# Performance work log

Measured on AMD Instinct MI355X. Metric: run time of the kernel, lower is better.

The kernel has to match this reference:

```python
import jax, jax.numpy as jnp
import numpy as np

B, LQ, D, H, L, P, DFF = 16, 1024, 256, 8, 4, 4, 1024
SHAPES = ((64, 64), (32, 32), (16, 16), (8, 8))  # (H_l, W_l) per level
LV = sum(h * w for h, w in SHAPES)  # 5440
DH = D // H
EPS = 1e-5


def layer_norm(x, g, b):
    m = jnp.mean(x, -1, keepdims=True)
    v = jnp.mean((x - m) ** 2, -1, keepdims=True)
    return (x - m) * jax.lax.rsqrt(v + EPS) * g + b


def mha(q_in, k_in, v_in, w, b, ow, ob):
    # torch nn.MultiheadAttention with packed in_proj [3D, D]
    q = (q_in @ w[:D].T + b[:D]).reshape(B, LQ, H, DH)
    k = (k_in @ w[D:2 * D].T + b[D:2 * D]).reshape(B, LQ, H, DH)
    v = (v_in @ w[2 * D:].T + b[2 * D:]).reshape(B, LQ, H, DH)
    a = jax.nn.softmax(jnp.einsum('bqhd,bkhd->bhqk', q, k) * (1.0 / np.sqrt(DH)), -1)
    o = jnp.einsum('bhqk,bkhd->bqhd', a, v).reshape(B, LQ, D)
    return o @ ow.T + ob


def ms_deform_attn(q, ref, src, value_w, value_b, off_w, off_b, attw_w, attw_b, outp_w, outp_b):
    # value: [B, H, LV, DH]
    value = (src @ value_w.T + value_b).reshape(B, LV, H, DH).transpose(0, 2, 1, 3)
    off = (q @ off_w.T + off_b).reshape(B, LQ, H, L, P, 2)
    attw = jax.nn.softmax((q @ attw_w.T + attw_b).reshape(B, LQ, H, L * P), -1).reshape(B, LQ, H, L, P)
    # offset normalizer = (W_l, H_l) matching (x, y) order of reference points
    normalizer = jnp.array([[w, h] for h, w in SHAPES], jnp.float32)
    loc = ref[:, :, None, :, None, :] + off / normalizer[None, None, None, :, None, :]  # [B,LQ,H,L,P,2]
    out = jnp.zeros((B, LQ, H, DH), jnp.float32)
    start = 0
    for l, (hl, wl) in enumerate(SHAPES):
        v = value[:, :, start:start + hl * wl]  # [B,H,N_l,DH]
        start += hl * wl
        # grid_sample semantics, align_corners=False, padding zeros
        x = loc[:, :, :, l, :, 0] * wl - 0.5  # [B,LQ,H,P]
        y = loc[:, :, :, l, :, 1] * hl - 0.5
        x0 = jnp.floor(x); y0 = jnp.floor(y)
        lx = (x - x0).transpose(0, 2, 1, 3)[..., None]  # [B,H,LQ,P,1]
        ly = (y - y0).transpose(0, 2, 1, 3)[..., None]
        x0i = x0.astype(jnp.int32); y0i = y0.astype(jnp.int32)

        def gather(xi, yi):
            valid = ((xi >= 0) & (xi < wl) & (yi >= 0) & (yi < hl)).astype(jnp.float32)
            idx = jnp.clip(yi, 0, hl - 1) * wl + jnp.clip(xi, 0, wl - 1)  # [B,LQ,H,P]
            idx2 = idx.transpose(0, 2, 1, 3).reshape(B, H, LQ * P)
            g = jnp.take_along_axis(v, jnp.broadcast_to(idx2[..., None], (B, H, LQ * P, DH)), axis=2)
            return g.reshape(B, H, LQ, P, DH) * valid.transpose(0, 2, 1, 3)[..., None]

        g00 = gather(x0i, y0i); g01 = gather(x0i + 1, y0i)
        g10 = gather(x0i, y0i + 1); g11 = gather(x0i + 1, y0i + 1)
        sampled = (g00 * (1 - lx) * (1 - ly) + g01 * lx * (1 - ly)
                   + g10 * (1 - lx) * ly + g11 * lx * ly)  # [B,H,LQ,P,DH]
        out = out + jnp.einsum('bhqpd,bqhp->bqhd', sampled, attw[:, :, :, l])
    return out.reshape(B, LQ, D) @ outp_w.T + outp_b


def setup_inputs() -> dict:
    key = jax.random.key(0)
    ks = jax.random.split(key, 16)
    s = 0.02
    inp = {}
    inp['tgt'] = jax.random.normal(ks[0], (B, LQ, D), jnp.float32)
    inp['query_pos'] = jax.random.normal(ks[1], (B, LQ, D), jnp.float32)
    inp['reference_points'] = jax.random.uniform(ks[2], (B, LQ, L, 2), jnp.float32)
    inp['src'] = jax.random.normal(ks[3], (B, LV, D), jnp.float32)
    # self-attention (MHA)
    inp['in_proj_w'] = jax.random.normal(ks[4], (3 * D, D), jnp.float32) * s
    inp['in_proj_b'] = jnp.zeros((3 * D,), jnp.float32)
    inp['out_proj_w'] = jax.random.normal(ks[5], (D, D), jnp.float32) * s
    inp['out_proj_b'] = jnp.zeros((D,), jnp.float32)
    inp['norm2_g'] = jnp.ones((D,), jnp.float32); inp['norm2_b'] = jnp.zeros((D,), jnp.float32)
    # MSDeformAttn
    inp['value_w'] = jax.random.normal(ks[6], (D, D), jnp.float32) * s
    inp['value_b'] = jnp.zeros((D,), jnp.float32)
    inp['off_w'] = jax.random.normal(ks[7], (H * L * P * 2, D), jnp.float32) * s
    inp['off_b'] = jax.random.normal(ks[8], (H * L * P * 2,), jnp.float32) * 0.5
    inp['attw_w'] = jax.random.normal(ks[9], (H * L * P, D), jnp.float32) * s
    inp['attw_b'] = jnp.zeros((H * L * P,), jnp.float32)
    inp['outp_w'] = jax.random.normal(ks[10], (D, D), jnp.float32) * s
    inp['outp_b'] = jnp.zeros((D,), jnp.float32)
    inp['norm1_g'] = jnp.ones((D,), jnp.float32); inp['norm1_b'] = jnp.zeros((D,), jnp.float32)
    # FFN
    inp['lin1_w'] = jax.random.normal(ks[11], (DFF, D), jnp.float32) * s
    inp['lin1_b'] = jnp.zeros((DFF,), jnp.float32)
    inp['lin2_w'] = jax.random.normal(ks[12], (D, DFF), jnp.float32) * s
    inp['lin2_b'] = jnp.zeros((D,), jnp.float32)
    inp['norm3_g'] = jnp.ones((D,), jnp.float32); inp['norm3_b'] = jnp.zeros((D,), jnp.float32)
    inp['src_spatial_shapes'] = jnp.array(SHAPES, jnp.int32)
    inp['level_start_index'] = jnp.array(np.concatenate([[0], np.cumsum([h * w for h, w in SHAPES[:-1]])]), jnp.int32)
    return inp


def reference(tgt, query_pos, reference_points, src,
              in_proj_w, in_proj_b, out_proj_w, out_proj_b, norm2_g, norm2_b,
              value_w, value_b, off_w, off_b, attw_w, attw_b, outp_w, outp_b,
              norm1_g, norm1_b, lin1_w, lin1_b, lin2_w, lin2_b, norm3_g, norm3_b,
              src_spatial_shapes, level_start_index):
    # dropout=0 (eval mode)
    q = tgt + query_pos
    tgt2 = mha(q, q, tgt, in_proj_w, in_proj_b, out_proj_w, out_proj_b)
    tgt = layer_norm(tgt + tgt2, norm2_g, norm2_b)
    tgt2 = ms_deform_attn(tgt + query_pos, reference_points, src,
                          value_w, value_b, off_w, off_b, attw_w, attw_b, outp_w, outp_b)
    tgt = layer_norm(tgt + tgt2, norm1_g, norm1_b)
    t2 = jax.nn.relu(tgt @ lin1_w.T + lin1_b) @ lin2_w.T + lin2_b
    return layer_norm(tgt + t2, norm3_g, norm3_b)
```

## Files before the change

### kernel.cpp

```cpp
#include <hip/hip_runtime.h>
#include <math.h>

typedef short s16x8 __attribute__((ext_vector_type(8)));
typedef float f32x4 __attribute__((ext_vector_type(4)));
typedef unsigned short u16;
typedef unsigned short u16x4 __attribute__((ext_vector_type(4)));

constexpr int cB    = 16;
constexpr int cLQ   = 1024;
constexpr int cD    = 256;
constexpr int cH    = 8;
constexpr int cLVTOT= 5440;
constexpr int cNTOK = cB * cLQ;
constexpr int cNV   = cB * cLVTOT;

__device__ __forceinline__ u16 f2b(float f) {
    __bf16 h = (__bf16)f;
    u16 u;
    __builtin_memcpy(&u, &h, 2);
    return u;
}
__device__ __forceinline__ float bl(unsigned x) {
    return __uint_as_float(x << 16);
}

__global__ __launch_bounds__(256) void cvt_kernel(const float4* __restrict__ in,
                                                  u16x4* __restrict__ out) {
    int i = blockIdx.x * 256 + threadIdx.x;
    float4 v = in[i];
    out[i] = (u16x4){ f2b(v.x), f2b(v.y), f2b(v.z), f2b(v.w) };
}

struct WArgs { const float4* src[8]; };
__global__ __launch_bounds__(256) void cvtw_kernel(WArgs a, u16x4* __restrict__ out) {
    int i = blockIdx.x * 256 + threadIdx.x;
    int s, off;
    if (i < 98304) {
        if (i < 65536) { if (i < 49152) { s = 0; off = i; } else { s = 1; off = i - 49152; } }
        else           { if (i < 81920) { s = 2; off = i - 65536; } else { s = 3; off = i - 81920; } }
    } else {
        if (i < 122880){ if (i < 106496){ s = 4; off = i - 98304; } else { s = 5; off = i - 106496; } }
        else           { if (i < 188416){ s = 6; off = i - 122880; } else { s = 7; off = i - 188416; } }
    }
    float4 v = a.src[s][off];
    out[i] = (u16x4){ f2b(v.x), f2b(v.y), f2b(v.z), f2b(v.w) };
}

__global__ __launch_bounds__(256) void prep_kernel(const float4* __restrict__ t,
                                                   const float4* __restrict__ q,
                                                   u16x4* __restrict__ tb,
                                                   u16x4* __restrict__ qb) {
    int i = blockIdx.x * 256 + threadIdx.x;
    float4 a = t[i], b = q[i];
    tb[i] = (u16x4){ f2b(a.x), f2b(a.y), f2b(a.z), f2b(a.w) };
    qb[i] = (u16x4){ f2b(a.x + b.x), f2b(a.y + b.y), f2b(a.z + b.z), f2b(a.w + b.w) };
}

template <int RELU, int OUTBF>
__global__ __launch_bounds__(256) void gemm_bf(const u16* __restrict__ A,
                                               const u16* __restrict__ Wt,
                                               const float* __restrict__ bias,
                                               float* __restrict__ Cf,
                                               u16* __restrict__ Cb,
                                               int M, int N, int K) {
    __shared__ u16 As[128 * 40];
    __shared__ u16 Bs[128 * 40];
    int tid = threadIdx.x;
    int bm = blockIdx.x * 128, bn = blockIdx.y * 128;
    int w = tid >> 6, lane = tid & 63, quad = lane >> 4, l15 = lane & 15;
    int wm = (w & 1) * 64, wn = (w >> 1) * 64;
    int r0 = tid >> 2, s0 = (tid & 3) * 8;
    f32x4 acc[16];
#pragma unroll
    for (int i = 0; i < 16; ++i) acc[i] = (f32x4){0.f, 0.f, 0.f, 0.f};
    for (int k0 = 0; k0 < K; k0 += 32) {
        __syncthreads();
        *(s16x8*)&As[r0 * 40 + s0]        = *(const s16x8*)(A  + (size_t)(bm + r0) * K + k0 + s0);
        *(s16x8*)&As[(r0 + 64) * 40 + s0] = *(const s16x8*)(A  + (size_t)(bm + r0 + 64) * K + k0 + s0);
        *(s16x8*)&Bs[r0 * 40 + s0]        = *(const s16x8*)(Wt + (size_t)(bn + r0) * K + k0 + s0);
        *(s16x8*)&Bs[(r0 + 64) * 40 + s0] = *(const s16x8*)(Wt + (size_t)(bn + r0 + 64) * K + k0 + s0);
        __syncthreads();
        s16x8 af[4], bf[4];
#pragma unroll
        for (int mt = 0; mt < 4; ++mt) af[mt] = *(const s16x8*)&As[(wm + mt * 16 + l15) * 40 + quad * 8];
#pragma unroll
        for (int nt = 0; nt < 4; ++nt) bf[nt] = *(const s16x8*)&Bs[(wn + nt * 16 + l15) * 40 + quad * 8];
#pragma unroll
        for (int mt = 0; mt < 4; ++mt)
#pragma unroll
            for (int nt = 0; nt < 4; ++nt)
                acc[mt * 4 + nt] = __builtin_amdgcn_mfma_f32_16x16x32_bf16(af[mt], bf[nt], acc[mt * 4 + nt], 0, 0, 0);
    }
    float bs[4];
#pragma unroll
    for (int nt = 0; nt < 4; ++nt) bs[nt] = bias[bn + wn + nt * 16 + l15];
#pragma unroll
    for (int mt = 0; mt < 4; ++mt) {
        int m = bm + wm + mt * 16 + quad * 4;
#pragma unroll
        for (int nt = 0; nt < 4; ++nt) {
            int n = bn + wn + nt * 16 + l15;
#pragma unroll
            for (int r = 0; r < 4; ++r) {
                float v = acc[mt * 4 + nt][r] + bs[nt];
                if (RELU) v = fmaxf(v, 0.f);
                if (OUTBF) Cb[(size_t)(m + r) * N + n] = f2b(v);
                else       Cf[(size_t)(m + r) * N + n] = v;
            }
        }
    }
}

__global__ __launch_bounds__(256) void vtrans_kernel(const u16* __restrict__ Vb,
                                                     u16* __restrict__ Vtg) {
    __shared__ u16 T[64 * 40];
    int tid = threadIdx.x;
    int tt = blockIdx.x & 15, bh = blockIdx.x >> 4;
    int h = bh & 7, b = bh >> 3;
    int r = tid >> 2, c = (tid & 3) * 8;
    *(s16x8*)&T[r * 40 + c] =
        *(const s16x8*)(Vb + (size_t)(b * cLQ + tt * 64 + r) * cD + h * 32 + c);
    __syncthreads();
    int dh = tid & 31, tc = (tid >> 5) * 8;
    s16x8 o;
#pragma unroll
    for (int i = 0; i < 8; ++i) o[i] = T[(tc + i) * 40 + dh];
    *(s16x8*)(Vtg + ((size_t)bh * 32 + dh) * cLQ + tt * 64 + tc) = o;
}

__global__ __launch_bounds__(256) void attn_mfma(const u16* __restrict__ Q,
                                                 const u16* __restrict__ K,
                                                 const u16* __restrict__ Vt,
                                                 u16* __restrict__ O) {
    __shared__ u16 Ks[64 * 40];
    __shared__ u16 Vs[32 * 72];
    __shared__ u16 Ps[4][16 * 72];
    int tid = threadIdx.x, w = tid >> 6, lane = tid & 63, quad = lane >> 4, l15 = lane & 15;
    int qt = blockIdx.x & 15, bh = blockIdx.x >> 4;
    int h = bh & 7, b = bh >> 3;
    int qbase = qt * 64 + w * 16;
    const float C = 0.25506734f;
    s16x8 qf = *(const s16x8*)(Q + (size_t)(b * cLQ + qbase + l15) * cD + h * 32 + quad * 8);
    f32x4 o0 = {0.f,0.f,0.f,0.f}, o1 = {0.f,0.f,0.f,0.f};
    float lsum = 0.f;
    int skey = tid >> 2, sdh = (tid & 3) * 8;
    int vdh = tid >> 3, vkc = (tid & 7) * 8;
    size_t kgbase = (size_t)(b * cLQ) * cD + h * 32;
    size_t vgbase = (size_t)bh * 32 * cLQ;
    for (int kt = 0; kt < cLQ; kt += 64) {
        __syncthreads();
        *(s16x8*)&Ks[skey * 40 + sdh] = *(const s16x8*)(K + kgbase + (size_t)(kt + skey) * cD + sdh);
        *(s16x8*)&Vs[vdh * 72 + vkc]  = *(const s16x8*)(Vt + vgbase + (size_t)vdh * cLQ + kt + vkc);
        __syncthreads();
#pragma unroll
        for (int t = 0; t < 4; ++t) {
            s16x8 kf = *(const s16x8*)&Ks[(t * 16 + l15) * 40 + quad * 8];
            f32x4 z = {0.f,0.f,0.f,0.f};
            f32x4 sc = __builtin_amdgcn_mfma_f32_16x16x32_bf16(kf, qf, z, 0, 0, 0);
            u16x4 pb;
#pragma unroll
            for (int r = 0; r < 4; ++r) {
                float p = exp2f(sc[r] * C);
                lsum += p;
                pb[r] = f2b(p);
            }
            *(u16x4*)&Ps[w][l15 * 72 + t * 16 + quad * 4] = pb;
        }
#pragma unroll
        for (int ks = 0; ks < 2; ++ks) {
            s16x8 pa  = *(const s16x8*)&Ps[w][l15 * 72 + ks * 32 + quad * 8];
            s16x8 vb0 = *(const s16x8*)&Vs[l15 * 72 + ks * 32 + quad * 8];
            s16x8 vb1 = *(const s16x8*)&Vs[(l15 + 16) * 72 + ks * 32 + quad * 8];
            o0 = __builtin_amdgcn_mfma_f32_16x16x32_bf16(pa, vb0, o0, 0, 0, 0);
            o1 = __builtin_amdgcn_mfma_f32_16x16x32_bf16(pa, vb1, o1, 0, 0, 0);
        }
    }
    lsum += __shfl_xor(lsum, 16);
    lsum += __shfl_xor(lsum, 32);
#pragma unroll
    for (int r = 0; r < 4; ++r) {
        float inv = 1.0f / __shfl(lsum, quad * 4 + r);
        int q = qbase + quad * 4 + r;
        size_t ob = (size_t)(b * cLQ + q) * cD + h * 32;
        O[ob + l15]      = f2b(o0[r] * inv);
        O[ob + 16 + l15] = f2b(o1[r] * inv);
    }
}

template <int WB, int QP>
__global__ __launch_bounds__(256) void add_ln_kernel(const float* __restrict__ X,
                                                     const float* __restrict__ R,
                                                     const float* __restrict__ g,
                                                     const float* __restrict__ bt,
                                                     const float* __restrict__ qp,
                                                     float* __restrict__ out,
                                                     u16* __restrict__ outb) {
    int wave = threadIdx.x / 64;
    int lane = threadIdx.x % 64;
    int row = blockIdx.x * 4 + wave;
    const float* x = X + (size_t)row * cD;
    const float* r = R + (size_t)row * cD;
    float4 xv = *(const float4*)(x + lane * 4);
    float4 rv = *(const float4*)(r + lane * 4);
    float v0 = xv.x + rv.x, v1 = xv.y + rv.y, v2 = xv.z + rv.z, v3 = xv.w + rv.w;
    float s = v0 + v1 + v2 + v3;
    float s2 = v0 * v0 + v1 * v1 + v2 * v2 + v3 * v3;
#pragma unroll
    for (int off = 32; off > 0; off >>= 1) {
        s += __shfl_xor(s, off);
        s2 += __shfl_xor(s2, off);
    }
    float mean = s * (1.0f / 256.0f);
    float var = s2 * (1.0f / 256.0f) - mean * mean;
    float rstd = rsqrtf(var + 1e-5f);
    float4 gv = *(const float4*)(g + lane * 4);
    float4 bv = *(const float4*)(bt + lane * 4);
    float4 o;
    o.x = (v0 - mean) * rstd * gv.x + bv.x;
    o.y = (v1 - mean) * rstd * gv.y + bv.y;
    o.z = (v2 - mean) * rstd * gv.z + bv.z;
    o.w = (v3 - mean) * rstd * gv.w + bv.w;
    *(float4*)(out + (size_t)row * cD + lane * 4) = o;
    if (WB) {
        u16x4 ob = { f2b(o.x), f2b(o.y), f2b(o.z), f2b(o.w) };
        *(u16x4*)(outb + (size_t)row * cD + lane * 4) = ob;
    }
    if (QP) {
        float4 qv = *(const float4*)(qp + (size_t)row * cD + lane * 4);
        u16x4 ob = { f2b(o.x + qv.x), f2b(o.y + qv.y), f2b(o.z + qv.z), f2b(o.w + qv.w) };
        *(u16x4*)(outb + (size_t)row * cD + lane * 4) = ob;
    }
}

__global__ __launch_bounds__(256) void deform_kernel(const u16* __restrict__ value,
                                                     const float* __restrict__ offb,
                                                     const float* __restrict__ attwl,
                                                     const float* __restrict__ refp,
                                                     u16* __restrict__ out) {
    int t = blockIdx.x * 32 + (threadIdx.x >> 3);
    int dq = threadIdx.x & 7;
    int h = t & 7;
    int bq = t >> 3;
    int b = bq >> 10;
    const float* al = attwl + (size_t)bq * 128 + h * 16;
    float wv[16];
    float mx = -1e30f;
#pragma unroll
    for (int i = 0; i < 16; ++i) { wv[i] = al[i]; mx = fmaxf(mx, wv[i]); }
    float sum = 0.f;
#pragma unroll
    for (int i = 0; i < 16; ++i) { wv[i] = __expf(wv[i] - mx); sum += wv[i]; }
    float inv = 1.f / sum;
    const float* off = offb + (size_t)bq * 256 + h * 32;
    const float* rp = refp + (size_t)bq * 8;
    const u16* vb = value + ((size_t)b * cLVTOT) * 256 + h * 32 + dq * 4;
    const int starts[4] = {0, 4096, 5120, 5376};
    const int dims[4] = {64, 32, 16, 8};
    float a0 = 0.f, a1 = 0.f, a2 = 0.f, a3 = 0.f;
#pragma unroll
    for (int l = 0; l < 4; ++l) {
        int hl = dims[l], wl = dims[l];
        float rx = rp[l * 2 + 0], ry = rp[l * 2 + 1];
#pragma unroll
        for (int p = 0; p < 4; ++p) {
            float ox = off[(l * 4 + p) * 2 + 0];
            float oy = off[(l * 4 + p) * 2 + 1];
            float x = rx * (float)wl + ox - 0.5f;
            float y = ry * (float)hl + oy - 0.5f;
            float x0f = floorf(x), y0f = floorf(y);
            float lx = x - x0f, ly = y - y0f;
            int x0 = (int)x0f, y0 = (int)y0f;
            float aw = wv[l * 4 + p] * inv;
            float cw[4] = {(1.f - lx) * (1.f - ly), lx * (1.f - ly),
                           (1.f - lx) * ly, lx * ly};
            int xs[4] = {x0, x0 + 1, x0, x0 + 1};
            int ys[4] = {y0, y0, y0 + 1, y0 + 1};
#pragma unroll
            for (int c = 0; c < 4; ++c) {
                int xi = xs[c], yi = ys[c];
                bool valid = (xi >= 0) && (xi < wl) && (yi >= 0) && (yi < hl);
                int xc = min(max(xi, 0), wl - 1);
                int yc = min(max(yi, 0), hl - 1);
                int idx = starts[l] + yc * wl + xc;
                float wgt = valid ? aw * cw[c] : 0.f;
                unsigned long long u = *(const unsigned long long*)(vb + (size_t)idx * 256);
                a0 += wgt * bl((unsigned)(u & 0xffffull));
                a1 += wgt * bl((unsigned)((u >> 16) & 0xffffull));
                a2 += wgt * bl((unsigned)((u >> 32) & 0xffffull));
                a3 += wgt * bl((unsigned)(u >> 48));
            }
        }
    }
    u16x4 o = { f2b(a0), f2b(a1), f2b(a2), f2b(a3) };
    *(u16x4*)(out + (size_t)bq * 256 + h * 32 + dq * 4) = o;
}

extern "C" void kernel_launch(void* const* d_in, const int* in_sizes, int n_in,
                              void* d_out, int out_size, void* d_ws, size_t ws_size,
                              hipStream_t stream) {
    const float* tgt        = (const float*)d_in[0];
    const float* query_pos  = (const float*)d_in[1];
    const float* refp       = (const float*)d_in[2];
    const float* src        = (const float*)d_in[3];
    const float* in_proj_w  = (const float*)d_in[4];
    const float* in_proj_b  = (const float*)d_in[5];
    const float* out_proj_w = (const float*)d_in[6];
    const float* out_proj_b = (const float*)d_in[7];
    const float* norm2_g    = (const float*)d_in[8];
    const float* norm2_b    = (const float*)d_in[9];
    const float* value_w    = (const float*)d_in[10];
    const float* value_b    = (const float*)d_in[11];
    const float* off_w      = (const float*)d_in[12];
    const float* off_b      = (const float*)d_in[13];
    const float* attw_w     = (const float*)d_in[14];
    const float* attw_b     = (const float*)d_in[15];
    const float* outp_w     = (const float*)d_in[16];
    const float* outp_b     = (const float*)d_in[17];
    const float* norm1_g    = (const float*)d_in[18];
    const float* norm1_b    = (const float*)d_in[19];
    const float* lin1_w     = (const float*)d_in[20];
    const float* lin1_b     = (const float*)d_in[21];
    const float* lin2_w     = (const float*)d_in[22];
    const float* lin2_b     = (const float*)d_in[23];
    const float* norm3_g    = (const float*)d_in[24];
    const float* norm3_b    = (const float*)d_in[25];

    char* W = (char*)d_ws;
    const size_t S84 = 8388608;
    u16*   tgtb  = (u16*)(W + 0);
    u16*   q2b   = (u16*)(W + 0);
    u16*   qb    = (u16*)(W + 1 * S84);
    float* attwf = (float*)(W + 1 * S84);
    u16*   Qb    = (u16*)(W + 2 * S84);
    u16*   dtb   = (u16*)(W + 2 * S84);
    u16*   Kb    = (u16*)(W + 3 * S84);
    u16*   x2b   = (u16*)(W + 3 * S84);
    u16*   Vb    = (u16*)(W + 4 * S84);
    float* ffn2f = (float*)(W + 4 * S84);
    u16*   aob   = (u16*)(W + 5 * S84);
    u16*   Vtg   = (u16*)(W + 6 * S84);
    float* t2f   = (float*)(W + 6 * S84);
    float* offf  = (float*)(W + 6 * S84);
    float* x1f   = (float*)(W + 8 * S84);
    float* x2f   = (float*)(W + 10 * S84);
    u16*   srcb  = (u16*)(W + 12 * S84);
    u16*   ffn1b = (u16*)(W + 12 * S84);
    u16*   valb  = (u16*)(W + 12 * S84 + 44564480);
    char*  wbase = W + 12 * S84 + 2 * 44564480;
    u16* wb_in   = (u16*)(wbase + 0);
    u16* wb_out  = (u16*)(wbase + 393216);
    u16* wb_val  = (u16*)(wbase + 524288);
    u16* wb_off  = (u16*)(wbase + 655360);
    u16* wb_attw = (u16*)(wbase + 786432);
    u16* wb_outp = (u16*)(wbase + 851968);
    u16* wb_lin1 = (u16*)(wbase + 983040);
    u16* wb_lin2 = (u16*)(wbase + 1507328);
    float* out = (float*)d_out;

    dim3 blk(256);

    prep_kernel<<<dim3(4096), blk, 0, stream>>>((const float4*)tgt, (const float4*)query_pos,
                                                (u16x4*)tgtb, (u16x4*)qb);
    WArgs wa;
    wa.src[0] = (const float4*)in_proj_w;  wa.src[1] = (const float4*)out_proj_w;
    wa.src[2] = (const float4*)value_w;    wa.src[3] = (const float4*)off_w;
    wa.src[4] = (const float4*)attw_w;     wa.src[5] = (const float4*)outp_w;
    wa.src[6] = (const float4*)lin1_w;     wa.src[7] = (const float4*)lin2_w;
    cvtw_kernel<<<dim3(992), blk, 0, stream>>>(wa, (u16x4*)wb_in);
    cvt_kernel<<<dim3(21760), blk, 0, stream>>>((const float4*)src, (u16x4*)srcb);

    gemm_bf<0, 1><<<dim3(128, 2), blk, 0, stream>>>(qb,   wb_in,             in_proj_b,       nullptr, Qb, cNTOK, 256, 256);
    gemm_bf<0, 1><<<dim3(128, 2), blk, 0, stream>>>(qb,   wb_in + 256 * 256, in_proj_b + 256, nullptr, Kb, cNTOK, 256, 256);
    gemm_bf<0, 1><<<dim3(128, 2), blk, 0, stream>>>(tgtb, wb_in + 512 * 256, in_proj_b + 512, nullptr, Vb, cNTOK, 256, 256);
    vtrans_kernel<<<dim3(2048), blk, 0, stream>>>(Vb, Vtg);
    attn_mfma<<<dim3(cB * cH * 16), blk, 0, stream>>>(Qb, Kb, Vtg, aob);
    gemm_bf<0, 0><<<dim3(128, 2), blk, 0, stream>>>(aob, wb_out, out_proj_b, t2f, nullptr, cNTOK, 256, 256);
    add_ln_kernel<0, 1><<<dim3(4096), blk, 0, stream>>>(tgt, t2f, norm2_g, norm2_b, query_pos, x1f, q2b);

    gemm_bf<0, 1><<<dim3(680, 2), blk, 0, stream>>>(srcb, wb_val, value_b, nullptr, valb, cNV, 256, 256);
    gemm_bf<0, 0><<<dim3(128, 2), blk, 0, stream>>>(q2b, wb_off,  off_b,  offf,  nullptr, cNTOK, 256, 256);
    gemm_bf<0, 0><<<dim3(128, 1), blk, 0, stream>>>(q2b, wb_attw, attw_b, attwf, nullptr, cNTOK, 128, 256);
    deform_kernel<<<dim3(4096), blk, 0, stream>>>(valb, offf, attwf, refp, dtb);
    gemm_bf<0, 0><<<dim3(128, 2), blk, 0, stream>>>(dtb, wb_outp, outp_b, t2f, nullptr, cNTOK, 256, 256);
    add_ln_kernel<1, 0><<<dim3(4096), blk, 0, stream>>>(x1f, t2f, norm1_g, norm1_b, nullptr, x2f, x2b);

    gemm_bf<1, 1><<<dim3(128, 8), blk, 0, stream>>>(x2b, wb_lin1, lin1_b, nullptr, ffn1b, cNTOK, 1024, 256);
    gemm_bf<0, 0><<<dim3(128, 2), blk, 0, stream>>>(ffn1b, wb_lin2, lin2_b, ffn2f, nullptr, cNTOK, 256, 1024);
    add_ln_kernel<0, 0><<<dim3(4096), blk, 0, stream>>>(x2f, ffn2f, norm3_g, norm3_b, nullptr, out, nullptr);
}
```

Measured before the change: 491.2 us.

## Use direct global-to-LDS loads, XOR-swizzled tiles, fused Q/K and offset/attw GEMMs

The GEMM rewrite loads tiles with global_load_lds straight into an unpadded, XOR-swizzled LDS layout, which removes register staging and bank conflicts. It also adds a 64-row GEMM variant so small-N GEMMs launch more blocks. Q and K projections are fused into one GEMM with N=512, and the offset and attention-weight projections are fused into one GEMM with N=384, using a concatenated bias copied on device. Attention LDS padding changes from 72 to 88, and attention and deform indexing are updated for the fused layouts. The fused offset/attw GEMM relies on the off and attw bf16 weights sitting next to each other in the weight buffer.

```diff
diff --git a/kernel.cpp b/kernel.cpp
--- a/kernel.cpp
+++ b/kernel.cpp
@@ -22,6 +22,10 @@
 }
 __device__ __forceinline__ float bl(unsigned x) {
     return __uint_as_float(x << 16);
+}
+__device__ __forceinline__ void load16(const u16* g, u16* l) {
+    __builtin_amdgcn_global_load_lds((const __attribute__((address_space(1))) void*)g,
+                                     (__attribute__((address_space(3))) void*)l, 16, 0, 0);
 }
 
 __global__ __launch_bounds__(256) void cvt_kernel(const float4* __restrict__ in,
@@ -57,34 +61,44 @@
 }
 
 template <int RELU, int OUTBF>
-__global__ __launch_bounds__(256) void gemm_bf(const u16* __restrict__ A,
+__global__ __launch_bounds__(256) void gemm128(const u16* __restrict__ A,
                                                const u16* __restrict__ Wt,
                                                const float* __restrict__ bias,
                                                float* __restrict__ Cf,
                                                u16* __restrict__ Cb,
                                                int M, int N, int K) {
-    __shared__ u16 As[128 * 40];
-    __shared__ u16 Bs[128 * 40];
+    __shared__ u16 As[128 * 32];
+    __shared__ u16 Bs[128 * 32];
     int tid = threadIdx.x;
     int bm = blockIdx.x * 128, bn = blockIdx.y * 128;
     int w = tid >> 6, lane = tid & 63, quad = lane >> 4, l15 = lane & 15;
     int wm = (w & 1) * 64, wn = (w >> 1) * 64;
-    int r0 = tid >> 2, s0 = (tid & 3) * 8;
+    int r0 = tid >> 2;
+    int c0 = ((tid & 3) ^ ((tid >> 3) & 3)) * 8;
+    const u16* ga0 = A  + (size_t)(bm + r0) * K + c0;
+    const u16* ga1 = ga0 + (size_t)64 * K;
+    const u16* gb0 = Wt + (size_t)(bn + r0) * K + c0;
+    const u16* gb1 = gb0 + (size_t)64 * K;
+    u16* la0 = As + (tid & 192) * 8;
+    u16* la1 = As + 64 * 32 + (tid & 192) * 8;
+    u16* lb0 = Bs + (tid & 192) * 8;
+    u16* lb1 = Bs + 64 * 32 + (tid & 192) * 8;
+    int abk = (quad ^ ((l15 >> 1) & 3)) * 8;
     f32x4 acc[16];
 #pragma unroll
     for (int i = 0; i < 16; ++i) acc[i] = (f32x4){0.f, 0.f, 0.f, 0.f};
     for (int k0 = 0; k0 < K; k0 += 32) {
         __syncthreads();
-        *(s16x8*)&As[r0 * 40 + s0]        = *(const s16x8*)(A  + (size_t)(bm + r0) * K + k0 + s0);
-        *(s16x8*)&As[(r0 + 64) * 40 + s0] = *(const s16x8*)(A  + (size_t)(bm + r0 + 64) * K + k0 + s0);
-        *(s16x8*)&Bs[r0 * 40 + s0]        = *(const s16x8*)(Wt + (size_t)(bn + r0) * K + k0 + s0);
-        *(s16x8*)&Bs[(r0 + 64) * 40 + s0] = *(const s16x8*)(Wt + (size_t)(bn + r0 + 64) * K + k0 + s0);
+        load16(ga0 + k0, la0);
+        load16(ga1 + k0, la1);
+        load16(gb0 + k0, lb0);
+        load16(gb1 + k0, lb1);
         __syncthreads();
         s16x8 af[4], bf[4];
 #pragma unroll
-        for (int mt = 0; mt < 4; ++mt) af[mt] = *(const s16x8*)&As[(wm + mt * 16 + l15) * 40 + quad * 8];
-#pragma unroll
-        for (int nt = 0; nt < 4; ++nt) bf[nt] = *(const s16x8*)&Bs[(wn + nt * 16 + l15) * 40 + quad * 8];
+        for (int mt = 0; mt < 4; ++mt) af[mt] = *(const s16x8*)&As[(wm + mt * 16 + l15) * 32 + abk];
+#pragma unroll
+        for (int nt = 0; nt < 4; ++nt) bf[nt] = *(const s16x8*)&Bs[(wn + nt * 16 + l15) * 32 + abk];
 #pragma unroll
         for (int mt = 0; mt < 4; ++mt)
 #pragma unroll
@@ -103,6 +117,68 @@
 #pragma unroll
             for (int r = 0; r < 4; ++r) {
                 float v = acc[mt * 4 + nt][r] + bs[nt];
+                if (RELU) v = fmaxf(v, 0.f);
+                if (OUTBF) Cb[(size_t)(m + r) * N + n] = f2b(v);
+                else       Cf[(size_t)(m + r) * N + n] = v;
+            }
+        }
+    }
+}
+
+template <int RELU, int OUTBF>
+__global__ __launch_bounds__(256) void gemm64(const u16* __restrict__ A,
+                                              const u16* __restrict__ Wt,
+                                              const float* __restrict__ bias,
+                                              float* __restrict__ Cf,
+                                              u16* __restrict__ Cb,
+                                              int M, int N, int K) {
+    __shared__ u16 As[64 * 32];
+    __shared__ u16 Bs[128 * 32];
+    int tid = threadIdx.x;
+    int bm = blockIdx.x * 64, bn = blockIdx.y * 128;
+    int w = tid >> 6, lane = tid & 63, quad = lane >> 4, l15 = lane & 15;
+    int wn = w * 32;
+    int r0 = tid >> 2;
+    int c0 = ((tid & 3) ^ ((tid >> 3) & 3)) * 8;
+    const u16* ga0 = A  + (size_t)(bm + r0) * K + c0;
+    const u16* gb0 = Wt + (size_t)(bn + r0) * K + c0;
+    const u16* gb1 = gb0 + (size_t)64 * K;
+    u16* la0 = As + (tid & 192) * 8;
+    u16* lb0 = Bs + (tid & 192) * 8;
+    u16* lb1 = Bs + 64 * 32 + (tid & 192) * 8;
+    int abk = (quad ^ ((l15 >> 1) & 3)) * 8;
+    f32x4 acc[8];
+#pragma unroll
+    for (int i = 0; i < 8; ++i) acc[i] = (f32x4){0.f, 0.f, 0.f, 0.f};
+    for (int k0 = 0; k0 < K; k0 += 32) {
+        __syncthreads();
+        load16(ga0 + k0, la0);
+        load16(gb0 + k0, lb0);
+        load16(gb1 + k0, lb1);
+        __syncthreads();
+        s16x8 af[4], bf[2];
+#pragma unroll
+        for (int mt = 0; mt < 4; ++mt) af[mt] = *(const s16x8*)&As[(mt * 16 + l15) * 32 + abk];
+#pragma unroll
+        for (int nt = 0; nt < 2; ++nt) bf[nt] = *(const s16x8*)&Bs[(wn + nt * 16 + l15) * 32 + abk];
+#pragma unroll
+        for (int mt = 0; mt < 4; ++mt)
+#pragma unroll
+            for (int nt = 0; nt < 2; ++nt)
+                acc[mt * 2 + nt] = __builtin_amdgcn_mfma_f32_16x16x32_bf16(af[mt], bf[nt], acc[mt * 2 + nt], 0, 0, 0);
+    }
+    float bs[2];
+#pragma unroll
+    for (int nt = 0; nt < 2; ++nt) bs[nt] = bias[bn + wn + nt * 16 + l15];
+#pragma unroll
+    for (int mt = 0; mt < 4; ++mt) {
+        int m = bm + mt * 16 + quad * 4;
+#pragma unroll
+        for (int nt = 0; nt < 2; ++nt) {
+            int n = bn + wn + nt * 16 + l15;
+#pragma unroll
+            for (int r = 0; r < 4; ++r) {
+                float v = acc[mt * 2 + nt][r] + bs[nt];
                 if (RELU) v = fmaxf(v, 0.f);
                 if (OUTBF) Cb[(size_t)(m + r) * N + n] = f2b(v);
                 else       Cf[(size_t)(m + r) * N + n] = v;
@@ -128,29 +204,28 @@
     *(s16x8*)(Vtg + ((size_t)bh * 32 + dh) * cLQ + tt * 64 + tc) = o;
 }
 
-__global__ __launch_bounds__(256) void attn_mfma(const u16* __restrict__ Q,
-                                                 const u16* __restrict__ K,
+__global__ __launch_bounds__(256) void attn_mfma(const u16* __restrict__ QK,
                                                  const u16* __restrict__ Vt,
                                                  u16* __restrict__ O) {
     __shared__ u16 Ks[64 * 40];
-    __shared__ u16 Vs[32 * 72];
-    __shared__ u16 Ps[4][16 * 72];
+    __shared__ u16 Vs[32 * 88];
+    __shared__ u16 Ps[4][16 * 88];
     int tid = threadIdx.x, w = tid >> 6, lane = tid & 63, quad = lane >> 4, l15 = lane & 15;
     int qt = blockIdx.x & 15, bh = blockIdx.x >> 4;
     int h = bh & 7, b = bh >> 3;
     int qbase = qt * 64 + w * 16;
     const float C = 0.25506734f;
-    s16x8 qf = *(const s16x8*)(Q + (size_t)(b * cLQ + qbase + l15) * cD + h * 32 + quad * 8);
+    s16x8 qf = *(const s16x8*)(QK + (size_t)(b * cLQ + qbase + l15) * 512 + h * 32 + quad * 8);
     f32x4 o0 = {0.f,0.f,0.f,0.f}, o1 = {0.f,0.f,0.f,0.f};
     float lsum = 0.f;
     int skey = tid >> 2, sdh = (tid & 3) * 8;
     int vdh = tid >> 3, vkc = (tid & 7) * 8;
-    size_t kgbase = (size_t)(b * cLQ) * cD + h * 32;
+    size_t kgbase = (size_t)(b * cLQ) * 512 + 256 + h * 32;
     size_t vgbase = (size_t)bh * 32 * cLQ;
     for (int kt = 0; kt < cLQ; kt += 64) {
         __syncthreads();
-        *(s16x8*)&Ks[skey * 40 + sdh] = *(const s16x8*)(K + kgbase + (size_t)(kt + skey) * cD + sdh);
-        *(s16x8*)&Vs[vdh * 72 + vkc]  = *(const s16x8*)(Vt + vgbase + (size_t)vdh * cLQ + kt + vkc);
+        *(s16x8*)&Ks[skey * 40 + sdh] = *(const s16x8*)(QK + kgbase + (size_t)(kt + skey) * 512 + sdh);
+        *(s16x8*)&Vs[vdh * 88 + vkc]  = *(const s16x8*)(Vt + vgbase + (size_t)vdh * cLQ + kt + vkc);
         __syncthreads();
 #pragma unroll
         for (int t = 0; t < 4; ++t) {
@@ -164,13 +239,13 @@
                 lsum += p;
                 pb[r] = f2b(p);
             }
-            *(u16x4*)&Ps[w][l15 * 72 + t * 16 + quad * 4] = pb;
+            *(u16x4*)&Ps[w][l15 * 88 + t * 16 + quad * 4] = pb;
         }
 #pragma unroll
         for (int ks = 0; ks < 2; ++ks) {
-            s16x8 pa  = *(const s16x8*)&Ps[w][l15 * 72 + ks * 32 + quad * 8];
-            s16x8 vb0 = *(const s16x8*)&Vs[l15 * 72 + ks * 32 + quad * 8];
-            s16x8 vb1 = *(const s16x8*)&Vs[(l15 + 16) * 72 + ks * 32 + quad * 8];
+            s16x8 pa  = *(const s16x8*)&Ps[w][l15 * 88 + ks * 32 + quad * 8];
+            s16x8 vb0 = *(const s16x8*)&Vs[l15 * 88 + ks * 32 + quad * 8];
+            s16x8 vb1 = *(const s16x8*)&Vs[(l15 + 16) * 88 + ks * 32 + quad * 8];
             o0 = __builtin_amdgcn_mfma_f32_16x16x32_bf16(pa, vb0, o0, 0, 0, 0);
             o1 = __builtin_amdgcn_mfma_f32_16x16x32_bf16(pa, vb1, o1, 0, 0, 0);
         }
@@ -233,8 +308,7 @@
 }
 
 __global__ __launch_bounds__(256) void deform_kernel(const u16* __restrict__ value,
-                                                     const float* __restrict__ offb,
-                                                     const float* __restrict__ attwl,
+                                                     const float* __restrict__ oa,
                                                      const float* __restrict__ refp,
                                                      u16* __restrict__ out) {
     int t = blockIdx.x * 32 + (threadIdx.x >> 3);
@@ -242,7 +316,7 @@
     int h = t & 7;
     int bq = t >> 3;
     int b = bq >> 10;
-    const float* al = attwl + (size_t)bq * 128 + h * 16;
+    const float* al = oa + (size_t)bq * 384 + 256 + h * 16;
     float wv[16];
     float mx = -1e30f;
 #pragma unroll
@@ -251,7 +325,7 @@
 #pragma unroll
     for (int i = 0; i < 16; ++i) { wv[i] = __expf(wv[i] - mx); sum += wv[i]; }
     float inv = 1.f / sum;
-    const float* off = offb + (size_t)bq * 256 + h * 32;
+    const float* off = oa + (size_t)bq * 384 + h * 32;
     const float* rp = refp + (size_t)bq * 8;
     const u16* vb = value + ((size_t)b * cLVTOT) * 256 + h * 32 + dq * 4;
     const int starts[4] = {0, 4096, 5120, 5376};
@@ -330,17 +404,15 @@
     u16*   tgtb  = (u16*)(W + 0);
     u16*   q2b   = (u16*)(W + 0);
     u16*   qb    = (u16*)(W + 1 * S84);
-    float* attwf = (float*)(W + 1 * S84);
-    u16*   Qb    = (u16*)(W + 2 * S84);
+    u16*   QKb   = (u16*)(W + 2 * S84);
     u16*   dtb   = (u16*)(W + 2 * S84);
-    u16*   Kb    = (u16*)(W + 3 * S84);
     u16*   x2b   = (u16*)(W + 3 * S84);
     u16*   Vb    = (u16*)(W + 4 * S84);
     float* ffn2f = (float*)(W + 4 * S84);
     u16*   aob   = (u16*)(W + 5 * S84);
+    float* oaf   = (float*)(W + 5 * S84);
     u16*   Vtg   = (u16*)(W + 6 * S84);
     float* t2f   = (float*)(W + 6 * S84);
-    float* offf  = (float*)(W + 6 * S84);
     float* x1f   = (float*)(W + 8 * S84);
     float* x2f   = (float*)(W + 10 * S84);
     u16*   srcb  = (u16*)(W + 12 * S84);
@@ -351,13 +423,16 @@
     u16* wb_out  = (u16*)(wbase + 393216);
     u16* wb_val  = (u16*)(wbase + 524288);
     u16* wb_off  = (u16*)(wbase + 655360);
-    u16* wb_attw = (u16*)(wbase + 786432);
     u16* wb_outp = (u16*)(wbase + 851968);
     u16* wb_lin1 = (u16*)(wbase + 983040);
     u16* wb_lin2 = (u16*)(wbase + 1507328);
+    float* biasoa= (float*)(wbase + 2031616);
     float* out = (float*)d_out;
 
     dim3 blk(256);
+
+    hipMemcpyAsync(biasoa,       off_b,  256 * 4, hipMemcpyDeviceToDevice, stream);
+    hipMemcpyAsync(biasoa + 256, attw_b, 128 * 4, hipMemcpyDeviceToDevice, stream);
 
     prep_kernel<<<dim3(4096), blk, 0, stream>>>((const float4*)tgt, (const float4*)query_pos,
                                                 (u16x4*)tgtb, (u16x4*)qb);
@@ -369,22 +444,20 @@
     cvtw_kernel<<<dim3(992), blk, 0, stream>>>(wa, (u16x4*)wb_in);
     cvt_kernel<<<dim3(21760), blk, 0, stream>>>((const float4*)src, (u16x4*)srcb);
 
-    gemm_bf<0, 1><<<dim3(128, 2), blk, 0, stream>>>(qb,   wb_in,             in_proj_b,       nullptr, Qb, cNTOK, 256, 256);
-    gemm_bf<0, 1><<<dim3(128, 2), blk, 0, stream>>>(qb,   wb_in + 256 * 256, in_proj_b + 256, nullptr, Kb, cNTOK, 256, 256);
-    gemm_bf<0, 1><<<dim3(128, 2), blk, 0, stream>>>(tgtb, wb_in + 512 * 256, in_proj_b + 512, nullptr, Vb, cNTOK, 256, 256);
+    gemm128<0, 1><<<dim3(128, 4), blk, 0, stream>>>(qb,   wb_in,             in_proj_b,       nullptr, QKb, cNTOK, 512, 256);
+    gemm64 <0, 1><<<dim3(256, 2), blk, 0, stream>>>(tgtb, wb_in + 512 * 256, in_proj_b + 512, nullptr, Vb,  cNTOK, 256, 256);
     vtrans_kernel<<<dim3(2048), blk, 0, stream>>>(Vb, Vtg);
-    attn_mfma<<<dim3(cB * cH * 16), blk, 0, stream>>>(Qb, Kb, Vtg, aob);
-    gemm_bf<0, 0><<<dim3(128, 2), blk, 0, stream>>>(aob, wb_out, out_proj_b, t2f, nullptr, cNTOK, 256, 256);
+    attn_mfma<<<dim3(cB * cH * 16), blk, 0, stream>>>(QKb, Vtg, aob);
+    gemm64 <0, 0><<<dim3(256, 2), blk, 0, stream>>>(aob, wb_out, out_proj_b, t2f, nullptr, cNTOK, 256, 256);
     add_ln_kernel<0, 1><<<dim3(4096), blk, 0, stream>>>(tgt, t2f, norm2_g, norm2_b, query_pos, x1f, q2b);
 
-    gemm_bf<0, 1><<<dim3(680, 2), blk, 0, stream>>>(srcb, wb_val, value_b, nullptr, valb, cNV, 256, 256);
-    gemm_bf<0, 0><<<dim3(128, 2), blk, 0, stream>>>(q2b, wb_off,  off_b,  offf,  nullptr, cNTOK, 256, 256);
-    gemm_bf<0, 0><<<dim3(128, 1), blk, 0, stream>>>(q2b, wb_attw, attw_b, attwf, nullptr, cNTOK, 128, 256);
-    deform_kernel<<<dim3(4096), blk, 0, stream>>>(valb, offf, attwf, refp, dtb);
-    gemm_bf<0, 0><<<dim3(128, 2), blk, 0, stream>>>(dtb, wb_outp, outp_b, t2f, nullptr, cNTOK, 256, 256);
+    gemm128<0, 1><<<dim3(680, 2), blk, 0, stream>>>(srcb, wb_val, value_b, nullptr, valb, cNV, 256, 256);
+    gemm64 <0, 0><<<dim3(256, 3), blk, 0, stream>>>(q2b, wb_off, biasoa, oaf, nullptr, cNTOK, 384, 256);
+    deform_kernel<<<dim3(4096), blk, 0, stream>>>(valb, oaf, refp, dtb);
+    gemm64 <0, 0><<<dim3(256, 2), blk, 0, stream>>>(dtb, wb_outp, outp_b, t2f, nullptr, cNTOK, 256, 256);
     add_ln_kernel<1, 0><<<dim3(4096), blk, 0, stream>>>(x1f, t2f, norm1_g, norm1_b, nullptr, x2f, x2b);
 
-    gemm_bf<1, 1><<<dim3(128, 8), blk, 0, stream>>>(x2b, wb_lin1, lin1_b, nullptr, ffn1b, cNTOK, 1024, 256);
-    gemm_bf<0, 0><<<dim3(128, 2), blk, 0, stream>>>(ffn1b, wb_lin2, lin2_b, ffn2f, nullptr, cNTOK, 256, 1024);
+    gemm128<1, 1><<<dim3(128, 8), blk, 0, stream>>>(x2b, wb_lin1, lin1_b, nullptr, ffn1b, cNTOK, 1024, 256);
+    gemm64 <0, 0><<<dim3(256, 2), blk, 0, stream>>>(ffn1b, wb_lin2, lin2_b, ffn2f, nullptr, cNTOK, 256, 1024);
     add_ln_kernel<0, 0><<<dim3(4096), blk, 0, stream>>>(x2f, ffn2f, norm3_g, norm3_b, nullptr, out, nullptr);
 }
```

After: 473.8 us. 3.6% less time.
